# Performance work log

Hardware: AMD Instinct MI355X
Metric: run time of the kernel (lower is better)

## Reference

```python
import jax, jax.numpy as jnp
import numpy as np

N_NODES = 100000
N_EDGES = 600000
D = 128          # input_dim
H = 256          # hidden_dim


def setup_inputs() -> dict:
    key = jax.random.key(0)
    k_emb, k_edge, k_w1, k_w2 = jax.random.split(key, 4)
    emd_all = jax.random.normal(k_emb, (N_NODES, D), dtype=jnp.float32)
    edge_index = jax.random.randint(k_edge, (N_EDGES, 2), 0, N_NODES, dtype=jnp.int32)
    # Linear(2*D, H) and Linear(H, 1); scale like torch default init ~ 1/sqrt(fan_in)
    W1 = jax.random.normal(k_w1, (2 * D, H), dtype=jnp.float32) / np.sqrt(2 * D)
    b1 = jnp.zeros((H,), dtype=jnp.float32)
    W2 = jax.random.normal(k_w2, (H, 1), dtype=jnp.float32) / np.sqrt(H)
    b2 = jnp.zeros((1,), dtype=jnp.float32)
    return {"emd_all": emd_all, "edge_index": edge_index,
            "W1": W1, "b1": b1, "W2": W2, "b2": b2}


def reference(emd_all, edge_index, W1, b1, W2, b2):
    # Gather source / destination node embeddings and concatenate: [E, 2*D]
    src = emd_all[edge_index[:, 0]]
    dst = emd_all[edge_index[:, 1]]
    edge_embeds = jnp.concatenate([src, dst], axis=-1)
    # 2-layer MLP classifier + sigmoid: [E, 1]
    h = jax.nn.relu(edge_embeds @ W1 + b1)
    logits = h @ W2 + b2
    link_predictions = jax.nn.sigmoid(logits)
    return link_predictions
```

## Files before the change

### kernel.cpp

```cpp
#include <hip/hip_runtime.h>
#include <hip/hip_bf16.h>

#define N_EDGES_C 600000
#define D_C 128

typedef __attribute__((ext_vector_type(8))) short short8;
typedef __attribute__((ext_vector_type(4))) float f32x4;

__device__ inline unsigned short f2bf(float f) {
    unsigned int u = __builtin_bit_cast(unsigned int, f);
    u += 0x7FFF + ((u >> 16) & 1);
    return (unsigned short)(u >> 16);
}

__device__ inline unsigned int pk2bf(float lo, float hi) {
    return (unsigned int)f2bf(lo) | ((unsigned int)f2bf(hi) << 16);
}

__global__ void prep_w1f(const float* __restrict__ W1, unsigned short* __restrict__ w1f) {
    int o = blockIdx.x * 256 + threadIdx.x;
    int j    = o & 7;
    int lane = (o >> 3) & 63;
    int kk   = (o >> 9) & 7;
    int nf   = o >> 12;
    int k = kk * 32 + (lane >> 4) * 8 + j;
    int n = nf * 16 + (lane & 15);
    w1f[o] = f2bf(W1[k * 256 + n]);
}

__global__ __launch_bounds__(256, 4) void edge_mlp(
    const float* __restrict__ emd,
    const int* __restrict__ eidx,
    const unsigned short* __restrict__ w1f,
    const float* __restrict__ b1,
    const float* __restrict__ W2,
    const float* __restrict__ b2,
    float* __restrict__ out)
{
    __shared__ unsigned char smem[32768];

    const int t    = threadIdx.x;
    const int lane = t & 63;
    const int wv   = t >> 6;
    const int rr   = lane & 15;
    const int lg   = lane >> 4;

    const int e0 = blockIdx.x * 64;

    {
        const int row = wv * 16 + rr;
        const int2 e2 = *reinterpret_cast<const int2*>(eidx + (size_t)(e0 + row) * 2);
        const float* ps = emd + (size_t)e2.x * D_C + lg * 4;
        const float* pd = emd + (size_t)e2.y * D_C + lg * 4;
        unsigned char* sw = smem + (wv * 8192 + (lg >> 1) * 256 + rr * 16 + (lg & 1) * 8);

        #pragma unroll
        for (int it = 0; it < 16; ++it) {
            const float* p = (it < 8) ? ps : pd;
            const float4 v = *reinterpret_cast<const float4*>(p + (it & 7) * 16);
            uint2 pk;
            pk.x = pk2bf(v.x, v.y);
            pk.y = pk2bf(v.z, v.w);
            *reinterpret_cast<uint2*>(sw + it * 512) = pk;
        }
    }
    __syncthreads();

    f32x4 acc[4][4];
    #pragma unroll
    for (int m = 0; m < 4; ++m)
        #pragma unroll
        for (int n4 = 0; n4 < 4; ++n4) acc[m][n4] = (f32x4){0.f, 0.f, 0.f, 0.f};

    #pragma unroll
    for (int kk = 0; kk < 8; ++kk) {
        short8 a[4];
        #pragma unroll
        for (int m = 0; m < 4; ++m)
            a[m] = *reinterpret_cast<const short8*>(smem + (m * 8 + kk) * 1024 + lane * 16);
        #pragma unroll
        for (int n4 = 0; n4 < 4; ++n4) {
            short8 b = *reinterpret_cast<const short8*>(
                w1f + ((size_t)((wv * 4 + n4) * 8 + kk) * 64 + lane) * 8);
            #pragma unroll
            for (int m = 0; m < 4; ++m)
                acc[m][n4] = __builtin_amdgcn_mfma_f32_16x16x32_bf16(a[m], b, acc[m][n4], 0, 0, 0);
        }
    }

    float pr[4][4];
    #pragma unroll
    for (int m = 0; m < 4; ++m)
        #pragma unroll
        for (int g = 0; g < 4; ++g) pr[m][g] = 0.f;

    #pragma unroll
    for (int n4 = 0; n4 < 4; ++n4) {
        int n = wv * 64 + n4 * 16 + rr;
        float b1v = b1[n];
        float w2v = W2[n];
        #pragma unroll
        for (int m = 0; m < 4; ++m)
            #pragma unroll
            for (int g = 0; g < 4; ++g) {
                float h = acc[m][n4][g] + b1v;
                h = h > 0.f ? h : 0.f;
                pr[m][g] += h * w2v;
            }
    }

    #pragma unroll
    for (int msk = 8; msk >= 1; msk >>= 1) {
        #pragma unroll
        for (int m = 0; m < 4; ++m)
            #pragma unroll
            for (int g = 0; g < 4; ++g)
                pr[m][g] += __shfl_xor(pr[m][g], msk, 64);
    }

    __syncthreads();
    float* partial = (float*)smem;

    if (rr == 0) {
        #pragma unroll
        for (int m = 0; m < 4; ++m)
            #pragma unroll
            for (int g = 0; g < 4; ++g)
                partial[wv * 64 + m * 16 + lg * 4 + g] = pr[m][g];
    }
    __syncthreads();

    if (t < 64) {
        float s = partial[t] + partial[64 + t] + partial[128 + t] + partial[192 + t] + b2[0];
        out[e0 + t] = 1.0f / (1.0f + __expf(-s));
    }
}

extern "C" void kernel_launch(void* const* d_in, const int* in_sizes, int n_in,
                              void* d_out, int out_size, void* d_ws, size_t ws_size,
                              hipStream_t stream) {
    const float* emd  = (const float*)d_in[0];
    const int*   eidx = (const int*)d_in[1];
    const float* W1   = (const float*)d_in[2];
    const float* b1   = (const float*)d_in[3];
    const float* W2   = (const float*)d_in[4];
    const float* b2   = (const float*)d_in[5];
    float* out = (float*)d_out;
    unsigned short* w1f = (unsigned short*)d_ws;

    prep_w1f<<<256, 256, 0, stream>>>(W1, w1f);

    const int nblocks = N_EDGES_C / 64;
    edge_mlp<<<nblocks, 256, 0, stream>>>(emd, eidx, w1f, b1, W2, b2, out);
}
```

Baseline: 162.5 us.

## Gather embedding rows with full-wave contiguous loads and XOR-swizzled LDS staging

Reworks the gather so each wave loads one edge's whole source and destination rows (32 lanes per row, 512 contiguous bytes) per iteration, replacing the scattered 16-byte per-lane row fetches. Each wave now handles rows p*4+wv instead of its own 16-row strip. LDS writes use an XOR swizzle of row index with k-chunk to avoid bank conflicts, and the MFMA A-operand reads apply the matching swizzle. This aims at better global coalescing during the gather, at the cost of 16 index loads per thread and more address arithmetic.

```diff
diff --git a/kernel.cpp b/kernel.cpp
--- a/kernel.cpp
+++ b/kernel.cpp
@@ -42,26 +42,29 @@
     const int t    = threadIdx.x;
     const int lane = t & 63;
     const int wv   = t >> 6;
-    const int rr   = lane & 15;
+    const int rr_c = lane & 15;
     const int lg   = lane >> 4;
 
     const int e0 = blockIdx.x * 64;
 
     {
-        const int row = wv * 16 + rr;
-        const int2 e2 = *reinterpret_cast<const int2*>(eidx + (size_t)(e0 + row) * 2);
-        const float* ps = emd + (size_t)e2.x * D_C + lg * 4;
-        const float* pd = emd + (size_t)e2.y * D_C + lg * 4;
-        unsigned char* sw = smem + (wv * 8192 + (lg >> 1) * 256 + rr * 16 + (lg & 1) * 8);
+        const int kk = lane >> 3;
+        const int kl = (lane >> 1) & 3;
+        const int lanepart = kk * 1024 + kl * 256 + (lane & 1) * 8;
+        const int f4 = lane & 31;
 
         #pragma unroll
-        for (int it = 0; it < 16; ++it) {
-            const float* p = (it < 8) ? ps : pd;
-            const float4 v = *reinterpret_cast<const float4*>(p + (it & 7) * 16);
+        for (int p = 0; p < 16; ++p) {
+            const int row = p * 4 + wv;
+            const int2 ep = *reinterpret_cast<const int2*>(eidx + (size_t)(e0 + row) * 2);
+            const int idx = (lane < 32) ? ep.x : ep.y;
+            const float4 v = *reinterpret_cast<const float4*>(emd + (size_t)idx * D_C + f4 * 4);
             uint2 pk;
             pk.x = pk2bf(v.x, v.y);
             pk.y = pk2bf(v.z, v.w);
-            *reinterpret_cast<uint2*>(sw + it * 512) = pk;
+            const int m  = row >> 4;
+            const int rr = row & 15;
+            *reinterpret_cast<uint2*>(smem + (m * 8192 + lanepart + ((rr ^ kk) << 4))) = pk;
         }
     }
     __syncthreads();
@@ -74,10 +77,11 @@
 
     #pragma unroll
     for (int kk = 0; kk < 8; ++kk) {
+        const int alow = ((lane & 48) | ((lane & 15) ^ kk)) << 4;
         short8 a[4];
         #pragma unroll
         for (int m = 0; m < 4; ++m)
-            a[m] = *reinterpret_cast<const short8*>(smem + (m * 8 + kk) * 1024 + lane * 16);
+            a[m] = *reinterpret_cast<const short8*>(smem + (m * 8 + kk) * 1024 + alow);
         #pragma unroll
         for (int n4 = 0; n4 < 4; ++n4) {
             short8 b = *reinterpret_cast<const short8*>(
@@ -96,7 +100,7 @@
 
     #pragma unroll
     for (int n4 = 0; n4 < 4; ++n4) {
-        int n = wv * 64 + n4 * 16 + rr;
+        int n = wv * 64 + n4 * 16 + rr_c;
         float b1v = b1[n];
         float w2v = W2[n];
         #pragma unroll
@@ -121,7 +125,7 @@
     __syncthreads();
     float* partial = (float*)smem;
 
-    if (rr == 0) {
+    if (rr_c == 0) {
         #pragma unroll
         for (int m = 0; m < 4; ++m)
             #pragma unroll
```

Measured after the change: 161.9 us. No clear change (-0.4%).
